# Kernel tuning notes

Hardware: AMD Instinct MI355X
Metric: run time of the kernel (lower is better)

## Reference

```python
import jax, jax.numpy as jnp
import numpy as np

CONNECTION_STRENGTH = 3.0   # hardcoded in AMN.forward
DIRECT_WEIGHT = 1.5         # direct_weight_initial
CONN_THRESHOLD = 0.1


def setup_inputs() -> dict:
    key = jax.random.key(0)
    k1, k2, k3, k4, k5 = jax.random.split(key, 5)
    U, T, N = 128, 256, 1024
    return {
        "input_spikes": (jax.random.uniform(k1, (T, N)) < 0.1).astype(jnp.float32),
        "unit_outputs": jax.random.uniform(k2, (U, T, N), dtype=jnp.float32),  # stacked ModularUnit outputs
        "conn": jax.random.uniform(k3, (U, U), dtype=jnp.float32),             # sampled connection matrix
        "target_spikes": (jax.random.uniform(k4, (T, N)) < 0.3).astype(jnp.float32),  # encode_number output
        "rand_bias": jax.random.uniform(k5, (T, N), dtype=jnp.float32),        # torch.rand_like for boost
    }


def reference(input_spikes, unit_outputs, conn, target_spikes, rand_bias):
    # get_spike_rate: mean firing rate in Hz (spikes.mean() * 1000)
    input_rate = input_spikes.mean() * 1000.0
    target_rate = input_rate + 20.0

    # Fused threshold-gated weighted aggregation:
    # for i,j: if conn[i,j] > 0.1: final += unit_outputs[j] * conn[i,j] * 3.0
    gated = jnp.where(conn > CONN_THRESHOLD, conn, 0.0)           # [U,U]
    w = CONNECTION_STRENGTH * gated.sum(axis=0)                   # [U] total inbound weight per source j
    final = jnp.einsum('j,jtn->tn', w, unit_outputs)              # [T,N]

    # Direct mapping heuristic
    final = final * 0.5 + target_spikes * DIRECT_WEIGHT

    # Conditional boost when mean activity is low
    mean = final.mean()
    target_mean = target_rate / 100.0
    boost = jnp.maximum(0.0, target_mean - mean)
    final = jnp.where(mean < 0.2, final + rand_bias * boost * 2.0, final)
    return final
```

## Files before the change

### kernel.cpp

```cpp
#include <hip/hip_runtime.h>

#define U    128
#define TN   (256 * 1024)
#define TN4  (TN / 4)
#define NBLK 256

typedef float vfloat4 __attribute__((ext_vector_type(4)));


__global__ __launch_bounds__(256) void fused_kernel(const float*   __restrict__ conn,
                                                    const vfloat4* __restrict__ uo,
                                                    const vfloat4* __restrict__ tgt,
                                                    const vfloat4* __restrict__ insp,
                                                    vfloat4*       __restrict__ out,
                                                    float*         __restrict__ ws) {
    __shared__ float wpart[2][U];
    __shared__ float w_s[U];
    int tid = threadIdx.x;

    {
        int j = tid & 127;
        int h = tid >> 7;
        const float* cp = conn + (size_t)(h * 64) * U + j;
        float s = 0.0f;
#pragma unroll
        for (int k = 0; k < 64; ++k) {
            float v = cp[(size_t)k * U];
            s += (v > 0.1f) ? v : 0.0f;
        }
        wpart[h][j] = s;
    }
    __syncthreads();
    if (tid < U) w_s[tid] = 3.0f * (wpart[0][tid] + wpart[1][tid]);
    __syncthreads();

    int idx = blockIdx.x * 256 + tid;
    const vfloat4* p = uo + idx;
    vfloat4 acc = 0.0f;
#pragma unroll 16
    for (int jj = 0; jj < U; ++jj)
        acc += w_s[jj] * __builtin_nontemporal_load(p + (size_t)jj * TN4);

    vfloat4 t = tgt[idx];
    vfloat4 r = acc * 0.5f + 1.5f * t;
    out[idx] = r;

    vfloat4 is = insp[idx];
    float lsum = r.x + r.y + r.z + r.w;
    float lin  = is.x + is.y + is.z + is.w;
#pragma unroll
    for (int off = 32; off > 0; off >>= 1) {
        lsum += __shfl_down(lsum, off, 64);
        lin  += __shfl_down(lin,  off, 64);
    }
    __shared__ float red[8];
    int wave = tid >> 6;
    int lane = tid & 63;
    if (lane == 0) { red[wave] = lsum; red[4 + wave] = lin; }
    __syncthreads();
    if (tid == 0) {
        ws[blockIdx.x]        = red[0] + red[1] + red[2] + red[3];
        ws[NBLK + blockIdx.x] = red[4] + red[5] + red[6] + red[7];
    }
}

__global__ __launch_bounds__(256) void boost_kernel(const vfloat4* __restrict__ rb,
                                                    vfloat4*       __restrict__ out,
                                                    const float*   __restrict__ ws) {
    int tid = threadIdx.x;
    float lsum = ws[tid];
    float lin  = ws[NBLK + tid];
#pragma unroll
    for (int off = 32; off > 0; off >>= 1) {
        lsum += __shfl_down(lsum, off, 64);
        lin  += __shfl_down(lin,  off, 64);
    }
    __shared__ float red[8];
    int wave = tid >> 6;
    int lane = tid & 63;
    if (lane == 0) { red[wave] = lsum; red[4 + wave] = lin; }
    __syncthreads();
    float tot = red[0] + red[1] + red[2] + red[3];
    float tin = red[4] + red[5] + red[6] + red[7];

    float mean        = tot * (1.0f / TN);
    float in_rate     = tin * (1000.0f / TN);
    float target_mean = (in_rate + 20.0f) * 0.01f;
    float boost       = fmaxf(0.0f, target_mean - mean);
    if (mean < 0.2f) {
        int idx = blockIdx.x * 256 + tid;
        out[idx] += rb[idx] * (boost * 2.0f);
    }
}

extern "C" void kernel_launch(void* const* d_in, const int* in_sizes, int n_in,
                              void* d_out, int out_size, void* d_ws, size_t ws_size,
                              hipStream_t stream) {
    const float* input_spikes = (const float*)d_in[0];
    const float* unit_outputs = (const float*)d_in[1];
    const float* conn         = (const float*)d_in[2];
    const float* target       = (const float*)d_in[3];
    const float* rand_bias    = (const float*)d_in[4];
    float* out = (float*)d_out;
    float* ws  = (float*)d_ws;

    fused_kernel<<<NBLK, 256, 0, stream>>>(
        conn, (const vfloat4*)unit_outputs, (const vfloat4*)target,
        (const vfloat4*)input_spikes, (vfloat4*)out, ws);

    boost_kernel<<<TN4 / 256, 256, 0, stream>>>(
        (const vfloat4*)rand_bias, (vfloat4*)out, ws);
}
```

Before: 192.8 us.

## Fuse boost pass into main kernel via cooperative grid sync

Merges the two kernels into one cooperative launch. A grid-wide sync follows the per-block partial reductions, so the boost can be applied to the value still in registers and the output is written once. This removes the second kernel launch and the read-modify-write of the output array. The target and input-spike loads are also moved ahead of the weight computation so they overlap with it. In exchange it depends on cooperative launch with all 256 blocks co-resident and pays for a grid barrier.

```diff
diff --git a/kernel.cpp b/kernel.cpp
--- a/kernel.cpp
+++ b/kernel.cpp
@@ -1,4 +1,7 @@
 #include <hip/hip_runtime.h>
+#include <hip/hip_cooperative_groups.h>
+
+namespace cg = cooperative_groups;
 
 #define U    128
 #define TN   (256 * 1024)
@@ -12,11 +15,17 @@
                                                     const vfloat4* __restrict__ uo,
                                                     const vfloat4* __restrict__ tgt,
                                                     const vfloat4* __restrict__ insp,
+                                                    const vfloat4* __restrict__ rb,
                                                     vfloat4*       __restrict__ out,
                                                     float*         __restrict__ ws) {
     __shared__ float wpart[2][U];
     __shared__ float w_s[U];
+    __shared__ float red[8];
     int tid = threadIdx.x;
+    int idx = blockIdx.x * 256 + tid;
+
+    vfloat4 t  = tgt[idx];
+    vfloat4 is = insp[idx];
 
     {
         int j = tid & 127;
@@ -34,18 +43,14 @@
     if (tid < U) w_s[tid] = 3.0f * (wpart[0][tid] + wpart[1][tid]);
     __syncthreads();
 
-    int idx = blockIdx.x * 256 + tid;
     const vfloat4* p = uo + idx;
     vfloat4 acc = 0.0f;
 #pragma unroll 16
     for (int jj = 0; jj < U; ++jj)
         acc += w_s[jj] * __builtin_nontemporal_load(p + (size_t)jj * TN4);
 
-    vfloat4 t = tgt[idx];
     vfloat4 r = acc * 0.5f + 1.5f * t;
-    out[idx] = r;
 
-    vfloat4 is = insp[idx];
     float lsum = r.x + r.y + r.z + r.w;
     float lin  = is.x + is.y + is.z + is.w;
 #pragma unroll
@@ -53,7 +58,6 @@
         lsum += __shfl_down(lsum, off, 64);
         lin  += __shfl_down(lin,  off, 64);
     }
-    __shared__ float red[8];
     int wave = tid >> 6;
     int lane = tid & 63;
     if (lane == 0) { red[wave] = lsum; red[4 + wave] = lin; }
@@ -62,23 +66,20 @@
         ws[blockIdx.x]        = red[0] + red[1] + red[2] + red[3];
         ws[NBLK + blockIdx.x] = red[4] + red[5] + red[6] + red[7];
     }
-}
+    __threadfence();
 
-__global__ __launch_bounds__(256) void boost_kernel(const vfloat4* __restrict__ rb,
-                                                    vfloat4*       __restrict__ out,
-                                                    const float*   __restrict__ ws) {
-    int tid = threadIdx.x;
-    float lsum = ws[tid];
-    float lin  = ws[NBLK + tid];
+    cg::this_grid().sync();
+
+    volatile const float* wsv = ws;
+    float a = wsv[tid];
+    float b = wsv[NBLK + tid];
 #pragma unroll
     for (int off = 32; off > 0; off >>= 1) {
-        lsum += __shfl_down(lsum, off, 64);
-        lin  += __shfl_down(lin,  off, 64);
+        a += __shfl_down(a, off, 64);
+        b += __shfl_down(b, off, 64);
     }
-    __shared__ float red[8];
-    int wave = tid >> 6;
-    int lane = tid & 63;
-    if (lane == 0) { red[wave] = lsum; red[4 + wave] = lin; }
+    __syncthreads();
+    if (lane == 0) { red[wave] = a; red[4 + wave] = b; }
     __syncthreads();
     float tot = red[0] + red[1] + red[2] + red[3];
     float tin = red[4] + red[5] + red[6] + red[7];
@@ -87,27 +88,28 @@
     float in_rate     = tin * (1000.0f / TN);
     float target_mean = (in_rate + 20.0f) * 0.01f;
     float boost       = fmaxf(0.0f, target_mean - mean);
-    if (mean < 0.2f) {
-        int idx = blockIdx.x * 256 + tid;
-        out[idx] += rb[idx] * (boost * 2.0f);
-    }
+    if (mean < 0.2f)
+        r += rb[idx] * (boost * 2.0f);
+
+    out[idx] = r;
 }
 
 extern "C" void kernel_launch(void* const* d_in, const int* in_sizes, int n_in,
                               void* d_out, int out_size, void* d_ws, size_t ws_size,
                               hipStream_t stream) {
-    const float* input_spikes = (const float*)d_in[0];
-    const float* unit_outputs = (const float*)d_in[1];
-    const float* conn         = (const float*)d_in[2];
-    const float* target       = (const float*)d_in[3];
-    const float* rand_bias    = (const float*)d_in[4];
-    float* out = (float*)d_out;
-    float* ws  = (float*)d_ws;
+    const float*   input_spikes = (const float*)d_in[0];
+    const vfloat4* unit_outputs = (const vfloat4*)d_in[1];
+    const float*   conn         = (const float*)d_in[2];
+    const vfloat4* target       = (const vfloat4*)d_in[3];
+    const vfloat4* rand_bias    = (const vfloat4*)d_in[4];
+    const vfloat4* insp4        = (const vfloat4*)input_spikes;
+    vfloat4* out = (vfloat4*)d_out;
+    float*   ws  = (float*)d_ws;
 
-    fused_kernel<<<NBLK, 256, 0, stream>>>(
-        conn, (const vfloat4*)unit_outputs, (const vfloat4*)target,
-        (const vfloat4*)input_spikes, (vfloat4*)out, ws);
-
-    boost_kernel<<<TN4 / 256, 256, 0, stream>>>(
-        (const vfloat4*)rand_bias, (vfloat4*)out, ws);
+    void* args[] = {
+        (void*)&conn, (void*)&unit_outputs, (void*)&target,
+        (void*)&insp4, (void*)&rand_bias, (void*)&out, (void*)&ws
+    };
+    hipLaunchCooperativeKernel((const void*)fused_kernel,
+                               dim3(NBLK), dim3(256), args, 0, stream);
 }
```

After: 278.4 us. +44.4%, slower.

## Fuse boost pass into main kernel with atomic-counter grid barrier

Applied to the files above, without the earlier changes.

Merges the second kernel into the first by adding a software grid-wide barrier: each block publishes its partial sums, increments an atomic counter and spins until all blocks arrive. Every block then reduces the global sums and applies the boost before writing the output once. This removes a kernel launch and the extra read-modify-write of the output. The barrier assumes the counter starts at a fixed poison value and is never reset, so it depends on the harness re-poisoning the workspace before each call. It also depends on all 256 blocks being co-resident.

```diff
diff --git a/kernel.cpp b/kernel.cpp
--- a/kernel.cpp
+++ b/kernel.cpp
@@ -7,16 +7,23 @@
 
 typedef float vfloat4 __attribute__((ext_vector_type(4)));
 
+#define POISON_U32 0xAAAAAAAAu
 
 __global__ __launch_bounds__(256) void fused_kernel(const float*   __restrict__ conn,
                                                     const vfloat4* __restrict__ uo,
                                                     const vfloat4* __restrict__ tgt,
                                                     const vfloat4* __restrict__ insp,
+                                                    const vfloat4* __restrict__ rb,
                                                     vfloat4*       __restrict__ out,
                                                     float*         __restrict__ ws) {
     __shared__ float wpart[2][U];
     __shared__ float w_s[U];
+    __shared__ float red[8];
     int tid = threadIdx.x;
+    int idx = blockIdx.x * 256 + tid;
+
+    vfloat4 t  = tgt[idx];
+    vfloat4 is = insp[idx];
 
     {
         int j = tid & 127;
@@ -34,18 +41,14 @@
     if (tid < U) w_s[tid] = 3.0f * (wpart[0][tid] + wpart[1][tid]);
     __syncthreads();
 
-    int idx = blockIdx.x * 256 + tid;
     const vfloat4* p = uo + idx;
     vfloat4 acc = 0.0f;
 #pragma unroll 16
     for (int jj = 0; jj < U; ++jj)
         acc += w_s[jj] * __builtin_nontemporal_load(p + (size_t)jj * TN4);
 
-    vfloat4 t = tgt[idx];
     vfloat4 r = acc * 0.5f + 1.5f * t;
-    out[idx] = r;
 
-    vfloat4 is = insp[idx];
     float lsum = r.x + r.y + r.z + r.w;
     float lin  = is.x + is.y + is.z + is.w;
 #pragma unroll
@@ -53,32 +56,33 @@
         lsum += __shfl_down(lsum, off, 64);
         lin  += __shfl_down(lin,  off, 64);
     }
-    __shared__ float red[8];
     int wave = tid >> 6;
     int lane = tid & 63;
     if (lane == 0) { red[wave] = lsum; red[4 + wave] = lin; }
     __syncthreads();
+
+    unsigned int* cnt = (unsigned int*)(ws + 512);
     if (tid == 0) {
-        ws[blockIdx.x]        = red[0] + red[1] + red[2] + red[3];
-        ws[NBLK + blockIdx.x] = red[4] + red[5] + red[6] + red[7];
+        __hip_atomic_store(&ws[blockIdx.x],        red[0] + red[1] + red[2] + red[3],
+                           __ATOMIC_RELAXED, __HIP_MEMORY_SCOPE_AGENT);
+        __hip_atomic_store(&ws[NBLK + blockIdx.x], red[4] + red[5] + red[6] + red[7],
+                           __ATOMIC_RELAXED, __HIP_MEMORY_SCOPE_AGENT);
+        __hip_atomic_fetch_add(cnt, 1u, __ATOMIC_RELEASE, __HIP_MEMORY_SCOPE_AGENT);
+        while ((__hip_atomic_load(cnt, __ATOMIC_ACQUIRE, __HIP_MEMORY_SCOPE_AGENT)
+                - POISON_U32) < (unsigned)NBLK) {
+            __builtin_amdgcn_s_sleep(1);
+        }
     }
-}
+    __syncthreads();
 
-__global__ __launch_bounds__(256) void boost_kernel(const vfloat4* __restrict__ rb,
-                                                    vfloat4*       __restrict__ out,
-                                                    const float*   __restrict__ ws) {
-    int tid = threadIdx.x;
-    float lsum = ws[tid];
-    float lin  = ws[NBLK + tid];
+    float a = __hip_atomic_load(&ws[tid],        __ATOMIC_RELAXED, __HIP_MEMORY_SCOPE_AGENT);
+    float b = __hip_atomic_load(&ws[NBLK + tid], __ATOMIC_RELAXED, __HIP_MEMORY_SCOPE_AGENT);
 #pragma unroll
     for (int off = 32; off > 0; off >>= 1) {
-        lsum += __shfl_down(lsum, off, 64);
-        lin  += __shfl_down(lin,  off, 64);
+        a += __shfl_down(a, off, 64);
+        b += __shfl_down(b, off, 64);
     }
-    __shared__ float red[8];
-    int wave = tid >> 6;
-    int lane = tid & 63;
-    if (lane == 0) { red[wave] = lsum; red[4 + wave] = lin; }
+    if (lane == 0) { red[wave] = a; red[4 + wave] = b; }
     __syncthreads();
     float tot = red[0] + red[1] + red[2] + red[3];
     float tin = red[4] + red[5] + red[6] + red[7];
@@ -87,10 +91,10 @@
     float in_rate     = tin * (1000.0f / TN);
     float target_mean = (in_rate + 20.0f) * 0.01f;
     float boost       = fmaxf(0.0f, target_mean - mean);
-    if (mean < 0.2f) {
-        int idx = blockIdx.x * 256 + tid;
-        out[idx] += rb[idx] * (boost * 2.0f);
-    }
+    if (mean < 0.2f)
+        r += rb[idx] * (boost * 2.0f);
+
+    out[idx] = r;
 }
 
 extern "C" void kernel_launch(void* const* d_in, const int* in_sizes, int n_in,
@@ -106,8 +110,6 @@
 
     fused_kernel<<<NBLK, 256, 0, stream>>>(
         conn, (const vfloat4*)unit_outputs, (const vfloat4*)target,
-        (const vfloat4*)input_spikes, (vfloat4*)out, ws);
-
-    boost_kernel<<<TN4 / 256, 256, 0, stream>>>(
-        (const vfloat4*)rand_bias, (vfloat4*)out, ws);
+        (const vfloat4*)input_spikes, (const vfloat4*)rand_bias,
+        (vfloat4*)out, ws);
 }
```

After: 214.6 us. +11.3%, slower.
